# Optimization experiments

Hardware: AMD Instinct MI355X
Metric: run time of the kernel (lower is better)

## Reference

```python
import jax, jax.numpy as jnp
import numpy as np

B = 2048          # number of graphs
NPG = 128         # nodes per graph (hard-coded by lin1 = Linear(128*hid, 1))
N = B * NPG       # total nodes = 262144
DEG = 16          # avg degree
EPG = NPG * DEG   # edges per graph
E = B * EPG       # total edges = 4194304
IN_CH = 151
HID = 64


def setup_inputs() -> dict:
    key = jax.random.key(0)
    ks = jax.random.split(key, 6)
    x = jax.random.normal(ks[0], (N, IN_CH), jnp.float32)
    # within-graph random edges: local index in [0, NPG) plus per-graph node offset
    src_loc = jax.random.randint(ks[1], (E,), 0, NPG, dtype=jnp.int32)
    dst_loc = jax.random.randint(ks[2], (E,), 0, NPG, dtype=jnp.int32)
    off = ((jnp.arange(E, dtype=jnp.int32) // EPG) * NPG)
    edge_index = jnp.stack([src_loc + off, dst_loc + off])  # [2, E] int32
    edge_weight = jax.random.uniform(ks[3], (E,), jnp.float32)
    batch = jnp.arange(N, dtype=jnp.int32) // NPG  # sorted graph ids
    W1 = jax.random.normal(ks[4], (IN_CH, HID), jnp.float32) / np.sqrt(IN_CH)
    b1 = jnp.zeros((HID,), jnp.float32)
    Wlin = jax.random.normal(ks[5], (NPG * HID, 1), jnp.float32) / np.sqrt(NPG * HID)
    blin = jnp.zeros((1,), jnp.float32)
    return {"x": x, "edge_index": edge_index, "edge_weight": edge_weight,
            "batch": batch, "W1": W1, "b1": b1, "Wlin": Wlin, "blin": blin}


def _gcn_conv(x, row, col, w, W, b, num_nodes):
    # PyG GCNConv: h = x @ W; out[col] += dinv[row]*w*dinv[col] * h[row]; out += b
    h = x @ W                                        # [N, HID]
    deg = jax.ops.segment_sum(w, col, num_segments=num_nodes)
    dinv = jnp.where(deg > 0, jax.lax.rsqrt(deg), 0.0)
    norm = dinv[row] * w * dinv[col]                 # [E+N]
    out = jax.ops.segment_sum(h[row] * norm[:, None], col, num_segments=num_nodes)
    return out + b


def reference(x, edge_index, edge_weight, batch, W1, b1, Wlin, blin):
    num_nodes = x.shape[0]
    # add self-loops with weight 1 (GCNConv default)
    sl = jnp.arange(num_nodes, dtype=edge_index.dtype)
    row = jnp.concatenate([edge_index[0], sl])
    col = jnp.concatenate([edge_index[1], sl])
    w = jnp.concatenate([edge_weight, jnp.ones((num_nodes,), x.dtype)])
    h = jax.nn.relu(_gcn_conv(x, row, col, w, W1, b1, num_nodes))  # [N, HID]
    # linearize: nodes are batch-sorted, 128 per graph -> [B, 128*HID]
    g = h.reshape(num_nodes // NPG, NPG * h.shape[1])
    return jax.nn.sigmoid(g @ Wlin + blin)  # [B, 1]
```

## Files before the change

### kernel.cpp

```cpp
#include <hip/hip_runtime.h>
#include <math.h>

#define NPG 128
#define HID 64
#define ICH 151
#define EPG 2048
#define TPB 512
#define EPT (EPG / TPB)
#define BTS 168
#define AS  136
#define HTS 136

typedef __attribute__((ext_vector_type(8))) short  short8;
typedef __attribute__((ext_vector_type(4))) float  floatx4;

static __device__ __forceinline__ unsigned short f2bf(float v) {
    unsigned u = __builtin_bit_cast(unsigned, v);
    return (unsigned short)((u + 0x7fffu + ((u >> 16) & 1u)) >> 16);
}

__global__ __launch_bounds__(TPB, 6) void gcn_fused(
    const float* __restrict__ x,
    const int*   __restrict__ erow,
    const int*   __restrict__ ecol,
    const float* __restrict__ ew,
    const float* __restrict__ W1,
    const float* __restrict__ b1,
    const float* __restrict__ Wlin,
    const float* __restrict__ blin,
    float* __restrict__ out)
{
    __shared__ __align__(16) float As[64 * AS];
    __shared__ __align__(16) short ht[HID * HTS];
    __shared__ float deg[NPG];
    __shared__ float dinv[NPG];
    __shared__ float red[TPB / 64];

    short* bt = (short*)As;

    const int t    = threadIdx.x;
    const int g    = blockIdx.x;
    const int lane = t & 63;
    const int wv   = t >> 6;
    const int c16  = lane & 15;
    const int kq   = (lane >> 4) * 8;

    if (t < NPG) deg[t] = 1.0f;
    {
        const int c  = t & 63;
        const int k0 = (t >> 6) * 2;
        for (int k = k0; k < BTS; k += 16) {
            float w0 = (k     < ICH) ? W1[k * HID + c]       : 0.0f;
            float w1 = (k + 1 < ICH) ? W1[(k + 1) * HID + c] : 0.0f;
            *(unsigned*)&bt[c * BTS + k] =
                (unsigned)f2bf(w0) | ((unsigned)f2bf(w1) << 16);
        }
    }
    short8 af[5];
    {
        const float* xr = x + (size_t)g * (NPG * ICH) + (wv * 16 + c16) * ICH;
        #pragma unroll
        for (int s = 0; s < 5; ++s) {
            #pragma unroll
            for (int j = 0; j < 8; ++j) {
                int k = s * 32 + kq + j;
                af[s][j] = (short)f2bf((k < ICH) ? xr[k] : 0.0f);
            }
        }
    }
    __syncthreads();

    const int ebase = g * EPG;
    #pragma unroll
    for (int it = 0; it < EPT; ++it) {
        int e = ebase + t + it * TPB;
        atomicAdd(&deg[ecol[e] & (NPG - 1)], ew[e]);
    }
    #pragma unroll
    for (int n = 0; n < 4; ++n) {
        floatx4 acc = {0.0f, 0.0f, 0.0f, 0.0f};
        #pragma unroll
        for (int s = 0; s < 5; ++s) {
            short8 b = *(const short8*)&bt[(n * 16 + c16) * BTS + s * 32 + kq];
            acc = __builtin_amdgcn_mfma_f32_16x16x32_bf16(af[s], b, acc, 0, 0, 0);
        }
        unsigned lo = (unsigned)f2bf(acc[0]) | ((unsigned)f2bf(acc[1]) << 16);
        unsigned hi = (unsigned)f2bf(acc[2]) | ((unsigned)f2bf(acc[3]) << 16);
        int col = n * 16 + c16;
        int row = wv * 16 + (lane >> 4) * 4;
        *(int2*)&ht[col * HTS + row] = make_int2((int)lo, (int)hi);
    }
    __syncthreads();

    if (t < NPG) dinv[t] = rsqrtf(deg[t]);
    __syncthreads();

    float partial = 0.0f;
    const int mrow = (wv >> 1) * 16 + c16;
    for (int half = 0; half < 2; ++half) {
        for (int z = t; z < 64 * AS / 4; z += TPB)
            ((floatx4*)As)[z] = (floatx4){0.0f, 0.0f, 0.0f, 0.0f};
        __syncthreads();

        #pragma unroll
        for (int it = 0; it < EPT; ++it) {
            int e  = ebase + t + it * TPB;
            int rl = erow[e] & (NPG - 1);
            int cl = ecol[e] & (NPG - 1);
            if ((cl >> 6) == half) {
                float nrm = dinv[rl] * ew[e] * dinv[cl];
                atomicAdd(&As[(cl & 63) * AS + rl], nrm);
            }
        }
        if (t < 64) {
            int i = half * 64 + t;
            atomicAdd(&As[t * AS + i], dinv[i] * dinv[i]);
        }
        __syncthreads();

        short8 afr[4];
        #pragma unroll
        for (int ks = 0; ks < 4; ++ks) {
            const float* ap = &As[mrow * AS + ks * 32 + kq];
            floatx4 a0 = *(const floatx4*)ap;
            floatx4 a1 = *(const floatx4*)(ap + 4);
            short8 v;
            v[0] = (short)f2bf(a0[0]); v[1] = (short)f2bf(a0[1]);
            v[2] = (short)f2bf(a0[2]); v[3] = (short)f2bf(a0[3]);
            v[4] = (short)f2bf(a1[0]); v[5] = (short)f2bf(a1[1]);
            v[6] = (short)f2bf(a1[2]); v[7] = (short)f2bf(a1[3]);
            afr[ks] = v;
        }
        #pragma unroll
        for (int nn = 0; nn < 2; ++nn) {
            int nt = (wv & 1) * 2 + nn;
            floatx4 acc = {0.0f, 0.0f, 0.0f, 0.0f};
            #pragma unroll
            for (int ks = 0; ks < 4; ++ks) {
                short8 b = *(const short8*)&ht[(nt * 16 + c16) * HTS + ks * 32 + kq];
                acc = __builtin_amdgcn_mfma_f32_16x16x32_bf16(afr[ks], b, acc, 0, 0, 0);
            }
            int col = nt * 16 + c16;
            float b1v = b1[col];
            int row0 = half * 64 + (wv >> 1) * 16 + (lane >> 4) * 4;
            #pragma unroll
            for (int r = 0; r < 4; ++r) {
                float v = fmaxf(acc[r] + b1v, 0.0f);
                partial += v * Wlin[(row0 + r) * HID + col];
            }
        }
        __syncthreads();
    }

    #pragma unroll
    for (int o = 32; o > 0; o >>= 1)
        partial += __shfl_down(partial, o, 64);
    if (lane == 0) red[wv] = partial;
    __syncthreads();
    if (t == 0) {
        float tot = blin[0];
        #pragma unroll
        for (int i = 0; i < TPB / 64; ++i) tot += red[i];
        out[g] = 1.0f / (1.0f + expf(-tot));
    }
}

extern "C" void kernel_launch(void* const* d_in, const int* in_sizes, int n_in,
                              void* d_out, int out_size, void* d_ws, size_t ws_size,
                              hipStream_t stream) {
    const float* x    = (const float*)d_in[0];
    const int*   ei   = (const int*)d_in[1];
    const float* ew   = (const float*)d_in[2];
    const float* W1   = (const float*)d_in[4];
    const float* b1   = (const float*)d_in[5];
    const float* Wlin = (const float*)d_in[6];
    const float* blin = (const float*)d_in[7];
    float* out = (float*)d_out;

    const int E = in_sizes[1] / 2;
    const int B = out_size;

    gcn_fused<<<B, TPB, 0, stream>>>(x, ei, ei + E, ew, W1, b1, Wlin, blin, out);
}
```

Measured before the change: 85.44 us.

## Split fused GCN kernel into GEMM and aggregation kernels via bf16 workspace

Splits the single fused kernel in two. The first kernel computes h = x@W1 in bf16, loading x with coalesced float4 reads into shared memory instead of strided scalar loads, and writes h to a global workspace. The second kernel handles degree and normalization, scatters into the adjacency, and reads h from global memory for the MFMA. Edge indices and weights are now cached in registers so they are not reloaded on each pass. The cost is an extra launch and a global write and read of h, in exchange for better-coalesced x loads and a smaller shared-memory footprint in the aggregation kernel.

After: 112.9 us. +32.2%, slower.

```diff
diff --git a/kernel.cpp b/kernel.cpp
--- a/kernel.cpp
+++ b/kernel.cpp
@@ -7,9 +7,10 @@
 #define EPG 2048
 #define TPB 512
 #define EPT (EPG / TPB)
+#define XSS 168
 #define BTS 168
-#define AS  136
 #define HTS 136
+#define AS  132
 
 typedef __attribute__((ext_vector_type(8))) short  short8;
 typedef __attribute__((ext_vector_type(4))) float  floatx4;
@@ -19,84 +20,121 @@
     return (unsigned short)((u + 0x7fffu + ((u >> 16) & 1u)) >> 16);
 }
 
-__global__ __launch_bounds__(TPB, 6) void gcn_fused(
-    const float* __restrict__ x,
+__global__ __launch_bounds__(TPB, 4) void gcn_gemm(
+    const float* __restrict__ x, const float* __restrict__ W1,
+    short* __restrict__ hg)
+{
+    __shared__ __align__(16) short xs[NPG * XSS];
+    __shared__ __align__(16) short bt[HID * BTS];
+    short* ht = xs;
+
+    const int t = threadIdx.x, g = blockIdx.x;
+    const int lane = t & 63, wv = t >> 6;
+    const int c16 = lane & 15, kq = (lane >> 4) * 8;
+
+    {
+        const int c = t & 63, k0 = (t >> 6) * 2;
+        for (int k = k0; k < BTS; k += 16) {
+            float w0 = (k     < ICH) ? W1[k * HID + c]       : 0.0f;
+            float w1 = (k + 1 < ICH) ? W1[(k + 1) * HID + c] : 0.0f;
+            *(unsigned*)&bt[c * BTS + k] =
+                (unsigned)f2bf(w0) | ((unsigned)f2bf(w1) << 16);
+        }
+    }
+    {
+        const float4* xg = (const float4*)(x + (size_t)g * (NPG * ICH));
+        for (int p = t; p < NPG * ICH / 4; p += TPB) {
+            float4 v = xg[p];
+            int e0 = p * 4;
+            #pragma unroll
+            for (int j = 0; j < 4; ++j) {
+                unsigned e = (unsigned)(e0 + j);
+                unsigned r = e / 151u, c = e - r * 151u;
+                xs[r * XSS + c] = (short)f2bf(((const float*)&v)[j]);
+            }
+        }
+        for (int idx = t; idx < NPG * 9; idx += TPB) {
+            int r = idx / 9, c = 151 + (idx - r * 9);
+            xs[r * XSS + c] = 0;
+        }
+    }
+    __syncthreads();
+
+    short8 af[5];
+    #pragma unroll
+    for (int s = 0; s < 5; ++s)
+        af[s] = *(const short8*)&xs[(wv * 16 + c16) * XSS + s * 32 + kq];
+    __syncthreads();
+
+    #pragma unroll
+    for (int n = 0; n < 4; ++n) {
+        floatx4 acc = {0.0f, 0.0f, 0.0f, 0.0f};
+        #pragma unroll
+        for (int s = 0; s < 5; ++s) {
+            short8 b = *(const short8*)&bt[(n * 16 + c16) * BTS + s * 32 + kq];
+            acc = __builtin_amdgcn_mfma_f32_16x16x32_bf16(af[s], b, acc, 0, 0, 0);
+        }
+        unsigned lo = (unsigned)f2bf(acc[0]) | ((unsigned)f2bf(acc[1]) << 16);
+        unsigned hi = (unsigned)f2bf(acc[2]) | ((unsigned)f2bf(acc[3]) << 16);
+        int col = n * 16 + c16;
+        int row = wv * 16 + (lane >> 4) * 4;
+        *(int2*)&ht[col * HTS + row] = make_int2((int)lo, (int)hi);
+    }
+    __syncthreads();
+
+    {
+        unsigned* dst = (unsigned*)(hg + (size_t)g * (HID * NPG));
+        #pragma unroll
+        for (int j = 0; j < 8; ++j) {
+            int p = t + j * TPB;
+            int ch = p >> 6, np = p & 63;
+            dst[ch * 64 + np] = *(const unsigned*)&ht[ch * HTS + 2 * np];
+        }
+    }
+}
+
+__global__ __launch_bounds__(TPB, 6) void gcn_agg(
     const int*   __restrict__ erow,
     const int*   __restrict__ ecol,
     const float* __restrict__ ew,
-    const float* __restrict__ W1,
+    const short* __restrict__ hg,
     const float* __restrict__ b1,
     const float* __restrict__ Wlin,
     const float* __restrict__ blin,
     float* __restrict__ out)
 {
     __shared__ __align__(16) float As[64 * AS];
-    __shared__ __align__(16) short ht[HID * HTS];
     __shared__ float deg[NPG];
     __shared__ float dinv[NPG];
     __shared__ float red[TPB / 64];
 
-    short* bt = (short*)As;
-
-    const int t    = threadIdx.x;
-    const int g    = blockIdx.x;
-    const int lane = t & 63;
-    const int wv   = t >> 6;
-    const int c16  = lane & 15;
-    const int kq   = (lane >> 4) * 8;
+    const int t = threadIdx.x, g = blockIdx.x;
+    const int lane = t & 63, wv = t >> 6;
+    const int c16 = lane & 15, kq = (lane >> 4) * 8;
 
     if (t < NPG) deg[t] = 1.0f;
-    {
-        const int c  = t & 63;
-        const int k0 = (t >> 6) * 2;
-        for (int k = k0; k < BTS; k += 16) {
-            float w0 = (k     < ICH) ? W1[k * HID + c]       : 0.0f;
-            float w1 = (k + 1 < ICH) ? W1[(k + 1) * HID + c] : 0.0f;
-            *(unsigned*)&bt[c * BTS + k] =
-                (unsigned)f2bf(w0) | ((unsigned)f2bf(w1) << 16);
-        }
-    }
-    short8 af[5];
-    {
-        const float* xr = x + (size_t)g * (NPG * ICH) + (wv * 16 + c16) * ICH;
-        #pragma unroll
-        for (int s = 0; s < 5; ++s) {
-            #pragma unroll
-            for (int j = 0; j < 8; ++j) {
-                int k = s * 32 + kq + j;
-                af[s][j] = (short)f2bf((k < ICH) ? xr[k] : 0.0f);
-            }
-        }
-    }
-    __syncthreads();
-
+    __syncthreads();
+
+    int   er_[EPT];
+    int   ec_[EPT];
+    float ew_[EPT];
     const int ebase = g * EPG;
     #pragma unroll
     for (int it = 0; it < EPT; ++it) {
         int e = ebase + t + it * TPB;
-        atomicAdd(&deg[ecol[e] & (NPG - 1)], ew[e]);
-    }
-    #pragma unroll
-    for (int n = 0; n < 4; ++n) {
-        floatx4 acc = {0.0f, 0.0f, 0.0f, 0.0f};
-        #pragma unroll
-        for (int s = 0; s < 5; ++s) {
-            short8 b = *(const short8*)&bt[(n * 16 + c16) * BTS + s * 32 + kq];
-            acc = __builtin_amdgcn_mfma_f32_16x16x32_bf16(af[s], b, acc, 0, 0, 0);
-        }
-        unsigned lo = (unsigned)f2bf(acc[0]) | ((unsigned)f2bf(acc[1]) << 16);
-        unsigned hi = (unsigned)f2bf(acc[2]) | ((unsigned)f2bf(acc[3]) << 16);
-        int col = n * 16 + c16;
-        int row = wv * 16 + (lane >> 4) * 4;
-        *(int2*)&ht[col * HTS + row] = make_int2((int)lo, (int)hi);
-    }
-    __syncthreads();
-
+        er_[it] = erow[e] & (NPG - 1);
+        ec_[it] = ecol[e] & (NPG - 1);
+        ew_[it] = ew[e];
+        atomicAdd(&deg[ec_[it]], ew_[it]);
+    }
+    __syncthreads();
     if (t < NPG) dinv[t] = rsqrtf(deg[t]);
     __syncthreads();
 
     float partial = 0.0f;
     const int mrow = (wv >> 1) * 16 + c16;
+    const short* hgg = hg + (size_t)g * (HID * NPG);
+
     for (int half = 0; half < 2; ++half) {
         for (int z = t; z < 64 * AS / 4; z += TPB)
             ((floatx4*)As)[z] = (floatx4){0.0f, 0.0f, 0.0f, 0.0f};
@@ -104,12 +142,10 @@
 
         #pragma unroll
         for (int it = 0; it < EPT; ++it) {
-            int e  = ebase + t + it * TPB;
-            int rl = erow[e] & (NPG - 1);
-            int cl = ecol[e] & (NPG - 1);
+            int cl = ec_[it];
             if ((cl >> 6) == half) {
-                float nrm = dinv[rl] * ew[e] * dinv[cl];
-                atomicAdd(&As[(cl & 63) * AS + rl], nrm);
+                int rl = er_[it];
+                atomicAdd(&As[(cl & 63) * AS + rl], dinv[rl] * ew_[it] * dinv[cl]);
             }
         }
         if (t < 64) {
@@ -137,7 +173,7 @@
             floatx4 acc = {0.0f, 0.0f, 0.0f, 0.0f};
             #pragma unroll
             for (int ks = 0; ks < 4; ++ks) {
-                short8 b = *(const short8*)&ht[(nt * 16 + c16) * HTS + ks * 32 + kq];
+                short8 b = *(const short8*)&hgg[(nt * 16 + c16) * NPG + ks * 32 + kq];
                 acc = __builtin_amdgcn_mfma_f32_16x16x32_bf16(afr[ks], b, acc, 0, 0, 0);
             }
             int col = nt * 16 + c16;
@@ -180,5 +216,8 @@
     const int E = in_sizes[1] / 2;
     const int B = out_size;
 
-    gcn_fused<<<B, TPB, 0, stream>>>(x, ei, ei + E, ew, W1, b1, Wlin, blin, out);
-}
+    short* hg = (short*)d_ws;
+
+    gcn_gemm<<<B, TPB, 0, stream>>>(x, W1, hg);
+    gcn_agg<<<B, TPB, 0, stream>>>(ei, ei + E, ew, hg, b1, Wlin, blin, out);
+}
```

## Stage x through LDS with coalesced float4 loads and cache edges in registers

Applied to the files above, without the earlier changes.

The x tile for each graph is now loaded with coalesced float4 reads and written as bf16 into a shared staging buffer, replacing strided per-thread scalar reads of rows. Edge indices and weights are loaded once into registers and the normalised weights are computed once, instead of re-reading global edge arrays in every pass. The adjacency aggregation now runs in four quarter passes over a smaller LDS buffer aliased with the weight tile, so the shared-memory footprint shrinks and more blocks can fit per CU. The cost is extra barriers, more passes over the edge list, and higher register pressure.

Result: slower. 94.71 us (+10.8%).

```diff
diff --git a/kernel.cpp b/kernel.cpp
--- a/kernel.cpp
+++ b/kernel.cpp
@@ -7,9 +7,11 @@
 #define EPG 2048
 #define TPB 512
 #define EPT (EPG / TPB)
+#define XSS 168
 #define BTS 168
-#define AS  136
 #define HTS 136
+#define ASS 132
+#define BT_OFF 21504
 
 typedef __attribute__((ext_vector_type(8))) short  short8;
 typedef __attribute__((ext_vector_type(4))) float  floatx4;
@@ -30,13 +32,15 @@
     const float* __restrict__ blin,
     float* __restrict__ out)
 {
-    __shared__ __align__(16) float As[64 * AS];
-    __shared__ __align__(16) short ht[HID * HTS];
+    __shared__ __align__(16) char smem[43008];
     __shared__ float deg[NPG];
     __shared__ float dinv[NPG];
     __shared__ float red[TPB / 64];
 
-    short* bt = (short*)As;
+    short* xs = (short*)smem;
+    short* ht = (short*)smem;
+    short* bt = (short*)(smem + BT_OFF);
+    float* As = (float*)(smem + BT_OFF);
 
     const int t    = threadIdx.x;
     const int g    = blockIdx.x;
@@ -45,10 +49,50 @@
     const int c16  = lane & 15;
     const int kq   = (lane >> 4) * 8;
 
+    int   er_[EPT];
+    int   ec_[EPT];
+    float nw_[EPT];
+    const int ebase = g * EPG;
+    #pragma unroll
+    for (int it = 0; it < EPT; ++it) {
+        int e = ebase + t + it * TPB;
+        er_[it] = erow[e] & (NPG - 1);
+        ec_[it] = ecol[e] & (NPG - 1);
+        nw_[it] = ew[e];
+    }
     if (t < NPG) deg[t] = 1.0f;
+
     {
-        const int c  = t & 63;
-        const int k0 = (t >> 6) * 2;
+        const float4* xg = (const float4*)(x + (size_t)g * (NPG * ICH));
+        for (int p = t; p < NPG * ICH / 4; p += TPB) {
+            float4 v = xg[p];
+            int e0 = 4 * p;
+            #pragma unroll
+            for (int j = 0; j < 4; ++j) {
+                unsigned e = (unsigned)(e0 + j);
+                unsigned r = e / 151u, c = e - 151u * r;
+                xs[r * XSS + c] = (short)f2bf(((const float*)&v)[j]);
+            }
+        }
+        for (int idx = t; idx < NPG * 9; idx += TPB) {
+            int r = idx / 9, c = ICH + (idx - 9 * r);
+            xs[r * XSS + c] = 0;
+        }
+    }
+    __syncthreads();
+
+    #pragma unroll
+    for (int it = 0; it < EPT; ++it)
+        atomicAdd(&deg[ec_[it]], nw_[it]);
+
+    short8 af[5];
+    #pragma unroll
+    for (int s = 0; s < 5; ++s)
+        af[s] = *(const short8*)&xs[(wv * 16 + c16) * XSS + s * 32 + kq];
+    __syncthreads();
+
+    {
+        const int c = t & 63, k0 = (t >> 6) * 2;
         for (int k = k0; k < BTS; k += 16) {
             float w0 = (k     < ICH) ? W1[k * HID + c]       : 0.0f;
             float w1 = (k + 1 < ICH) ? W1[(k + 1) * HID + c] : 0.0f;
@@ -56,26 +100,13 @@
                 (unsigned)f2bf(w0) | ((unsigned)f2bf(w1) << 16);
         }
     }
-    short8 af[5];
-    {
-        const float* xr = x + (size_t)g * (NPG * ICH) + (wv * 16 + c16) * ICH;
-        #pragma unroll
-        for (int s = 0; s < 5; ++s) {
-            #pragma unroll
-            for (int j = 0; j < 8; ++j) {
-                int k = s * 32 + kq + j;
-                af[s][j] = (short)f2bf((k < ICH) ? xr[k] : 0.0f);
-            }
-        }
-    }
-    __syncthreads();
-
-    const int ebase = g * EPG;
-    #pragma unroll
-    for (int it = 0; it < EPT; ++it) {
-        int e = ebase + t + it * TPB;
-        atomicAdd(&deg[ecol[e] & (NPG - 1)], ew[e]);
-    }
+    if (t < NPG) dinv[t] = rsqrtf(deg[t]);
+    __syncthreads();
+
+    #pragma unroll
+    for (int it = 0; it < EPT; ++it)
+        nw_[it] = dinv[er_[it]] * nw_[it] * dinv[ec_[it]];
+
     #pragma unroll
     for (int n = 0; n < 4; ++n) {
         floatx4 acc = {0.0f, 0.0f, 0.0f, 0.0f};
@@ -92,62 +123,48 @@
     }
     __syncthreads();
 
-    if (t < NPG) dinv[t] = rsqrtf(deg[t]);
-    __syncthreads();
-
     float partial = 0.0f;
-    const int mrow = (wv >> 1) * 16 + c16;
-    for (int half = 0; half < 2; ++half) {
-        for (int z = t; z < 64 * AS / 4; z += TPB)
-            ((floatx4*)As)[z] = (floatx4){0.0f, 0.0f, 0.0f, 0.0f};
+    const int mt  = wv >> 2;
+    const int nt  = wv & 3;
+    const int col = nt * 16 + c16;
+    const float b1v = b1[col];
+
+    for (int q = 0; q < 4; ++q) {
+        for (int p = t; p < 32 * ASS / 4; p += TPB)
+            ((floatx4*)As)[p] = (floatx4){0.0f, 0.0f, 0.0f, 0.0f};
         __syncthreads();
 
         #pragma unroll
         for (int it = 0; it < EPT; ++it) {
-            int e  = ebase + t + it * TPB;
-            int rl = erow[e] & (NPG - 1);
-            int cl = ecol[e] & (NPG - 1);
-            if ((cl >> 6) == half) {
-                float nrm = dinv[rl] * ew[e] * dinv[cl];
-                atomicAdd(&As[(cl & 63) * AS + rl], nrm);
-            }
-        }
-        if (t < 64) {
-            int i = half * 64 + t;
-            atomicAdd(&As[t * AS + i], dinv[i] * dinv[i]);
+            int cl = ec_[it];
+            if ((cl >> 5) == q)
+                atomicAdd(&As[(cl & 31) * ASS + er_[it]], nw_[it]);
+        }
+        if (t < 32) {
+            int i = q * 32 + t;
+            atomicAdd(&As[t * ASS + i], dinv[i] * dinv[i]);
         }
         __syncthreads();
 
-        short8 afr[4];
+        floatx4 acc = {0.0f, 0.0f, 0.0f, 0.0f};
         #pragma unroll
         for (int ks = 0; ks < 4; ++ks) {
-            const float* ap = &As[mrow * AS + ks * 32 + kq];
+            const float* ap = &As[(mt * 16 + c16) * ASS + ks * 32 + kq];
             floatx4 a0 = *(const floatx4*)ap;
             floatx4 a1 = *(const floatx4*)(ap + 4);
-            short8 v;
-            v[0] = (short)f2bf(a0[0]); v[1] = (short)f2bf(a0[1]);
-            v[2] = (short)f2bf(a0[2]); v[3] = (short)f2bf(a0[3]);
-            v[4] = (short)f2bf(a1[0]); v[5] = (short)f2bf(a1[1]);
-            v[6] = (short)f2bf(a1[2]); v[7] = (short)f2bf(a1[3]);
-            afr[ks] = v;
-        }
-        #pragma unroll
-        for (int nn = 0; nn < 2; ++nn) {
-            int nt = (wv & 1) * 2 + nn;
-            floatx4 acc = {0.0f, 0.0f, 0.0f, 0.0f};
-            #pragma unroll
-            for (int ks = 0; ks < 4; ++ks) {
-                short8 b = *(const short8*)&ht[(nt * 16 + c16) * HTS + ks * 32 + kq];
-                acc = __builtin_amdgcn_mfma_f32_16x16x32_bf16(afr[ks], b, acc, 0, 0, 0);
-            }
-            int col = nt * 16 + c16;
-            float b1v = b1[col];
-            int row0 = half * 64 + (wv >> 1) * 16 + (lane >> 4) * 4;
-            #pragma unroll
-            for (int r = 0; r < 4; ++r) {
-                float v = fmaxf(acc[r] + b1v, 0.0f);
-                partial += v * Wlin[(row0 + r) * HID + col];
-            }
+            short8 av;
+            av[0] = (short)f2bf(a0[0]); av[1] = (short)f2bf(a0[1]);
+            av[2] = (short)f2bf(a0[2]); av[3] = (short)f2bf(a0[3]);
+            av[4] = (short)f2bf(a1[0]); av[5] = (short)f2bf(a1[1]);
+            av[6] = (short)f2bf(a1[2]); av[7] = (short)f2bf(a1[3]);
+            short8 b = *(const short8*)&ht[col * HTS + ks * 32 + kq];
+            acc = __builtin_amdgcn_mfma_f32_16x16x32_bf16(av, b, acc, 0, 0, 0);
+        }
+        int node0 = q * 32 + mt * 16 + (lane >> 4) * 4;
+        #pragma unroll
+        for (int r = 0; r < 4; ++r) {
+            float v = fmaxf(acc[r] + b1v, 0.0f);
+            partial += v * Wlin[(node0 + r) * HID + col];
         }
         __syncthreads();
     }
```

## Stage x tiles into LDS via async global_load_lds and keep W1 in registers

Applied to the files above, without the earlier changes.

Replaces the strided per-thread scalar loads of x rows with coalesced global_load_lds copies into an LDS staging buffer. The buffer is processed in four 32-node quarters and the next quarter's load is issued while the current one computes. W1 fragments now live in registers per wave, so the LDS transpose of W1 goes away. Edge indices and weights are loaded once into registers and the normalized weights are computed once, which removes the second global pass over edges. Register pressure rises and there are extra barriers per quarter, which could hurt occupancy under the 6-blocks launch bound.

New measurement: 119.6 us. +40.0%, slower.

```diff
diff --git a/kernel.cpp b/kernel.cpp
--- a/kernel.cpp
+++ b/kernel.cpp
@@ -7,16 +7,33 @@
 #define EPG 2048
 #define TPB 512
 #define EPT (EPG / TPB)
-#define BTS 168
-#define AS  136
+#define QR  32
+#define XSS 156
 #define HTS 136
+#define ASS 132
+#define HT_BYTES 17408
+#define STG_CHUNKS ((QR * XSS) / 64)
 
 typedef __attribute__((ext_vector_type(8))) short  short8;
 typedef __attribute__((ext_vector_type(4))) float  floatx4;
+
+typedef const __attribute__((address_space(1))) void GV;
+typedef __attribute__((address_space(3))) void LV;
 
 static __device__ __forceinline__ unsigned short f2bf(float v) {
     unsigned u = __builtin_bit_cast(unsigned, v);
     return (unsigned short)((u + 0x7fffu + ((u >> 16) & 1u)) >> 16);
+}
+static __device__ __forceinline__ short8 pack2(floatx4 a, floatx4 b) {
+    short8 r;
+    r[0] = (short)f2bf(a[0]); r[1] = (short)f2bf(a[1]);
+    r[2] = (short)f2bf(a[2]); r[3] = (short)f2bf(a[3]);
+    r[4] = (short)f2bf(b[0]); r[5] = (short)f2bf(b[1]);
+    r[6] = (short)f2bf(b[2]); r[7] = (short)f2bf(b[3]);
+    return r;
+}
+static __device__ __forceinline__ void ld_lds4(const float* src, float* lds_base) {
+    __builtin_amdgcn_global_load_lds((GV*)src, (LV*)lds_base, 4, 0, 0);
 }
 
 __global__ __launch_bounds__(TPB, 6) void gcn_fused(
@@ -30,13 +47,14 @@
     const float* __restrict__ blin,
     float* __restrict__ out)
 {
-    __shared__ __align__(16) float As[64 * AS];
-    __shared__ __align__(16) short ht[HID * HTS];
+    __shared__ __align__(16) char smem[HT_BYTES + 64 * ASS * 4];
     __shared__ float deg[NPG];
     __shared__ float dinv[NPG];
     __shared__ float red[TPB / 64];
 
-    short* bt = (short*)As;
+    short* ht = (short*)smem;
+    float* xs = (float*)(smem + HT_BYTES);
+    float* As = (float*)(smem + HT_BYTES);
 
     const int t    = threadIdx.x;
     const int g    = blockIdx.x;
@@ -46,107 +64,140 @@
     const int kq   = (lane >> 4) * 8;
 
     if (t < NPG) deg[t] = 1.0f;
-    {
-        const int c  = t & 63;
-        const int k0 = (t >> 6) * 2;
-        for (int k = k0; k < BTS; k += 16) {
-            float w0 = (k     < ICH) ? W1[k * HID + c]       : 0.0f;
-            float w1 = (k + 1 < ICH) ? W1[(k + 1) * HID + c] : 0.0f;
-            *(unsigned*)&bt[c * BTS + k] =
-                (unsigned)f2bf(w0) | ((unsigned)f2bf(w1) << 16);
-        }
-    }
-    short8 af[5];
-    {
-        const float* xr = x + (size_t)g * (NPG * ICH) + (wv * 16 + c16) * ICH;
-        #pragma unroll
-        for (int s = 0; s < 5; ++s) {
-            #pragma unroll
-            for (int j = 0; j < 8; ++j) {
-                int k = s * 32 + kq + j;
-                af[s][j] = (short)f2bf((k < ICH) ? xr[k] : 0.0f);
-            }
-        }
-    }
-    __syncthreads();
-
+
+    int   er_[EPT];
+    int   ec_[EPT];
+    float nw_[EPT];
     const int ebase = g * EPG;
     #pragma unroll
     for (int it = 0; it < EPT; ++it) {
         int e = ebase + t + it * TPB;
-        atomicAdd(&deg[ecol[e] & (NPG - 1)], ew[e]);
-    }
-    #pragma unroll
-    for (int n = 0; n < 4; ++n) {
+        er_[it] = erow[e] & (NPG - 1);
+        ec_[it] = ecol[e] & (NPG - 1);
+        nw_[it] = ew[e];
+    }
+
+    short8 bf[5];
+    {
+        const int ch = (wv & 3) * 16 + c16;
+        #pragma unroll
+        for (int s = 0; s < 5; ++s) {
+            short8 v;
+            #pragma unroll
+            for (int j = 0; j < 8; ++j) {
+                int k = s * 32 + kq + j;
+                v[j] = (short)f2bf((k < ICH) ? W1[k * HID + ch] : 0.0f);
+            }
+            bf[s] = v;
+        }
+    }
+
+    const float* xg = x + (size_t)g * (NPG * ICH);
+    for (int i = wv; i < STG_CHUNKS; i += 8) {
+        int p = i * 64 + lane;
+        unsigned r = (unsigned)p / 156u;
+        unsigned c = (unsigned)p - 156u * r;
+        ld_lds4(xg + r * ICH + (c < (unsigned)ICH ? c : 0u), xs + i * 64);
+    }
+
+    const int mq  = wv >> 2;
+    const int chO = (wv & 3) * 16 + c16;
+    for (int q = 0; q < 4; ++q) {
+        __syncthreads();
+        short8 af[5];
+        {
+            const float* xrow = xs + (mq * 16 + c16) * XSS;
+            #pragma unroll
+            for (int s = 0; s < 4; ++s) {
+                floatx4 a0 = *(const floatx4*)(xrow + s * 32 + kq);
+                floatx4 a1 = *(const floatx4*)(xrow + s * 32 + kq + 4);
+                af[s] = pack2(a0, a1);
+            }
+            if (kq < 16) {
+                floatx4 a0 = *(const floatx4*)(xrow + 128 + kq);
+                floatx4 a1 = *(const floatx4*)(xrow + 132 + kq);
+                af[4] = pack2(a0, a1);
+            } else if (kq == 16) {
+                floatx4 a0 = *(const floatx4*)(xrow + 144);
+                floatx4 a1 = {xrow[148], xrow[149], xrow[150], 0.0f};
+                af[4] = pack2(a0, a1);
+            } else {
+                af[4] = (short8){0, 0, 0, 0, 0, 0, 0, 0};
+            }
+        }
+        __syncthreads();
+        if (q < 3) {
+            const float* xq = xg + (q + 1) * (QR * ICH);
+            for (int i = wv; i < STG_CHUNKS; i += 8) {
+                int p = i * 64 + lane;
+                unsigned r = (unsigned)p / 156u;
+                unsigned c = (unsigned)p - 156u * r;
+                ld_lds4(xq + r * ICH + (c < (unsigned)ICH ? c : 0u), xs + i * 64);
+            }
+        }
+        if (q == 0) {
+            #pragma unroll
+            for (int it = 0; it < EPT; ++it)
+                atomicAdd(&deg[ec_[it]], nw_[it]);
+        }
         floatx4 acc = {0.0f, 0.0f, 0.0f, 0.0f};
         #pragma unroll
-        for (int s = 0; s < 5; ++s) {
-            short8 b = *(const short8*)&bt[(n * 16 + c16) * BTS + s * 32 + kq];
-            acc = __builtin_amdgcn_mfma_f32_16x16x32_bf16(af[s], b, acc, 0, 0, 0);
-        }
-        unsigned lo = (unsigned)f2bf(acc[0]) | ((unsigned)f2bf(acc[1]) << 16);
-        unsigned hi = (unsigned)f2bf(acc[2]) | ((unsigned)f2bf(acc[3]) << 16);
-        int col = n * 16 + c16;
-        int row = wv * 16 + (lane >> 4) * 4;
-        *(int2*)&ht[col * HTS + row] = make_int2((int)lo, (int)hi);
+        for (int s = 0; s < 5; ++s)
+            acc = __builtin_amdgcn_mfma_f32_16x16x32_bf16(af[s], bf[s], acc, 0, 0, 0);
+        int node0 = q * QR + mq * 16 + (lane >> 4) * 4;
+        *(int2*)&ht[chO * HTS + node0] = make_int2(
+            (int)((unsigned)f2bf(acc[0]) | ((unsigned)f2bf(acc[1]) << 16)),
+            (int)((unsigned)f2bf(acc[2]) | ((unsigned)f2bf(acc[3]) << 16)));
     }
     __syncthreads();
 
     if (t < NPG) dinv[t] = rsqrtf(deg[t]);
     __syncthreads();
+    #pragma unroll
+    for (int it = 0; it < EPT; ++it)
+        nw_[it] = dinv[er_[it]] * nw_[it] * dinv[ec_[it]];
 
     float partial = 0.0f;
     const int mrow = (wv >> 1) * 16 + c16;
     for (int half = 0; half < 2; ++half) {
-        for (int z = t; z < 64 * AS / 4; z += TPB)
-            ((floatx4*)As)[z] = (floatx4){0.0f, 0.0f, 0.0f, 0.0f};
+        for (int p = t; p < 64 * ASS / 4; p += TPB)
+            ((floatx4*)As)[p] = (floatx4){0.0f, 0.0f, 0.0f, 0.0f};
         __syncthreads();
 
         #pragma unroll
         for (int it = 0; it < EPT; ++it) {
-            int e  = ebase + t + it * TPB;
-            int rl = erow[e] & (NPG - 1);
-            int cl = ecol[e] & (NPG - 1);
-            if ((cl >> 6) == half) {
-                float nrm = dinv[rl] * ew[e] * dinv[cl];
-                atomicAdd(&As[(cl & 63) * AS + rl], nrm);
-            }
+            int cl = ec_[it];
+            if ((cl >> 6) == half)
+                atomicAdd(&As[(cl & 63) * ASS + er_[it]], nw_[it]);
         }
         if (t < 64) {
             int i = half * 64 + t;
-            atomicAdd(&As[t * AS + i], dinv[i] * dinv[i]);
+            atomicAdd(&As[t * ASS + i], dinv[i] * dinv[i]);
         }
         __syncthreads();
 
         short8 afr[4];
         #pragma unroll
         for (int ks = 0; ks < 4; ++ks) {
-            const float* ap = &As[mrow * AS + ks * 32 + kq];
-            floatx4 a0 = *(const floatx4*)ap;
-            floatx4 a1 = *(const floatx4*)(ap + 4);
-            short8 v;
-            v[0] = (short)f2bf(a0[0]); v[1] = (short)f2bf(a0[1]);
-            v[2] = (short)f2bf(a0[2]); v[3] = (short)f2bf(a0[3]);
-            v[4] = (short)f2bf(a1[0]); v[5] = (short)f2bf(a1[1]);
-            v[6] = (short)f2bf(a1[2]); v[7] = (short)f2bf(a1[3]);
-            afr[ks] = v;
+            const float* ap = &As[mrow * ASS + ks * 32 + kq];
+            afr[ks] = pack2(*(const floatx4*)ap, *(const floatx4*)(ap + 4));
         }
         #pragma unroll
         for (int nn = 0; nn < 2; ++nn) {
-            int nt = (wv & 1) * 2 + nn;
+            int nt2 = (wv & 1) * 2 + nn;
             floatx4 acc = {0.0f, 0.0f, 0.0f, 0.0f};
             #pragma unroll
             for (int ks = 0; ks < 4; ++ks) {
-                short8 b = *(const short8*)&ht[(nt * 16 + c16) * HTS + ks * 32 + kq];
+                short8 b = *(const short8*)&ht[(nt2 * 16 + c16) * HTS + ks * 32 + kq];
                 acc = __builtin_amdgcn_mfma_f32_16x16x32_bf16(afr[ks], b, acc, 0, 0, 0);
             }
-            int col = nt * 16 + c16;
+            int col = nt2 * 16 + c16;
             float b1v = b1[col];
-            int row0 = half * 64 + (wv >> 1) * 16 + (lane >> 4) * 4;
+            int node0 = half * 64 + (wv >> 1) * 16 + (lane >> 4) * 4;
             #pragma unroll
             for (int r = 0; r < 4; ++r) {
                 float v = fmaxf(acc[r] + b1v, 0.0f);
-                partial += v * Wlin[(row0 + r) * HID + col];
+                partial += v * Wlin[(node0 + r) * HID + col];
             }
         }
         __syncthreads();
```
